# Kernel tuning notes

Measured on AMD Instinct MI355X. Metric: run time of the kernel, lower is better.

## Reference

```python
import jax, jax.numpy as jnp
import numpy as np

H = 128        # num_hidden
NIN = 384      # num_in
FF = 4 * H
SCALE = 30.0
EPS = 1e-5


def _gelu(x):
    return jax.nn.gelu(x, approximate=False)


def _layernorm(x, g, b):
    mu = jnp.mean(x, axis=-1, keepdims=True)
    var = jnp.var(x, axis=-1, keepdims=True)
    return (x - mu) * jax.lax.rsqrt(var + EPS) * g + b


def setup_inputs() -> dict:
    key = jax.random.key(0)
    ks = jax.random.split(key, 12)
    B, N, K = 4, 2048, 48
    s = lambda fan_in: 1.0 / np.sqrt(fan_in)
    inp = {
        "h_V": jax.random.normal(ks[0], (B, N, H), jnp.float32),
        "h_E": jax.random.normal(ks[1], (B, N, K, NIN), jnp.float32),
        "mask_V": jnp.ones((B, N), jnp.float32),
        "mask_attend": jnp.ones((B, N, K), jnp.float32),
        "W1_w": jax.random.uniform(ks[2], (H + NIN, H), jnp.float32, -s(H + NIN), s(H + NIN)),
        "W1_b": jnp.zeros((H,), jnp.float32),
        "W2_w": jax.random.uniform(ks[3], (H, H), jnp.float32, -s(H), s(H)),
        "W2_b": jnp.zeros((H,), jnp.float32),
        "W3_w": jax.random.uniform(ks[4], (H, H), jnp.float32, -s(H), s(H)),
        "W3_b": jnp.zeros((H,), jnp.float32),
        "Win_w": jax.random.uniform(ks[5], (H, FF), jnp.float32, -s(H), s(H)),
        "Win_b": jnp.zeros((FF,), jnp.float32),
        "Wout_w": jax.random.uniform(ks[6], (FF, H), jnp.float32, -s(FF), s(FF)),
        "Wout_b": jnp.zeros((H,), jnp.float32),
        "ln1_g": jnp.ones((H,), jnp.float32),
        "ln1_b": jnp.zeros((H,), jnp.float32),
        "ln2_g": jnp.ones((H,), jnp.float32),
        "ln2_b": jnp.zeros((H,), jnp.float32),
    }
    return inp


def reference(h_V, h_E, mask_V, mask_attend,
              W1_w, W1_b, W2_w, W2_b, W3_w, W3_b,
              Win_w, Win_b, Wout_w, Wout_b,
              ln1_g, ln1_b, ln2_g, ln2_b):
    B, N, K, _ = h_E.shape
    # expand node feats over K neighbors and concat with edge feats -> [B,N,K,H+NIN]
    h_V_expand = jnp.broadcast_to(h_V[:, :, None, :], (B, N, K, h_V.shape[-1]))
    h_EV = jnp.concatenate([h_V_expand, h_E], axis=-1)
    # edge MLP: 3 linears, 2 GELUs
    h_message = _gelu(h_EV @ W1_w + W1_b)
    h_message = _gelu(h_message @ W2_w + W2_b)
    h_message = h_message @ W3_w + W3_b
    h_message = mask_attend[..., None] * h_message
    dh = jnp.sum(h_message, axis=-2) / SCALE  # [B,N,H]
    h = _layernorm(h_V + dh, ln1_g, ln1_b)
    # position-wise FFN
    dh = _gelu(h @ Win_w + Win_b) @ Wout_w + Wout_b
    h = _layernorm(h + dh, ln2_g, ln2_b)
    h = mask_V[..., None] * h
    return h
```

## Files before the change

kernel.cpp:

```cpp
#include <hip/hip_runtime.h>
#include <hip/hip_bf16.h>

#define Hh    128
#define NINc  384
#define KN    48
#define FFd   512
#define NNODE 8192

typedef __attribute__((ext_vector_type(8))) short short8v;
typedef __attribute__((ext_vector_type(4))) float f32x4;

__device__ __forceinline__ short f2bf1(float f){
  union { __hip_bfloat16 h; short s; } c; c.h = __float2bfloat16(f);
  return c.s;
}
__device__ __forceinline__ unsigned pk_bf16(float lo, float hi){
  union { __hip_bfloat162 h; unsigned u; } c;
  c.h = __float22bfloat162_rn(make_float2(lo, hi));
  return c.u;
}

__device__ __forceinline__ float gelu_f(float x){
  float t = 0.7978845608028654f * x * (1.0f + 0.044715f * x * x);
  float e = __expf(2.0f * t);
  return x * (1.0f - 1.0f / (e + 1.0f));
}

__device__ __forceinline__ void bar_lds(){
  asm volatile("s_waitcnt lgkmcnt(0)\n\ts_barrier" ::: "memory");
}

__global__ void prep_weights(const float* __restrict__ W1, const float* __restrict__ W2,
                             const float* __restrict__ W3, const float* __restrict__ Win,
                             const float* __restrict__ Wout,
                             short* __restrict__ w1vT, short* __restrict__ w1p,
                             short* __restrict__ w2p,  short* __restrict__ w3T,
                             short* __restrict__ winT, short* __restrict__ woutT)
{
  int i = blockIdx.x * 256 + threadIdx.x;
  if (i < 16384){ int n = i / 128, k = i % 128; w1vT[i] = f2bf1(W1[k*128 + n]); return; }
  i -= 16384;
  if (i < 49152){
    int n = i / 6144, r = i % 6144;
    int ks = r / 512, r2 = r % 512;
    int lane = r2 / 8, j = r2 % 8;
    int qq = lane >> 4, arow = lane & 15;
    w1p[i] = f2bf1(W1[(128 + ks*32 + qq*8 + j)*128 + n*16 + arow]); return;
  }
  i -= 49152;
  if (i < 16384){
    int n = i / 2048, r = i % 2048;
    int ks = r / 512, r2 = r % 512;
    int lane = r2 / 8, j = r2 % 8;
    int qq = lane >> 4, arow = lane & 15;
    w2p[i] = f2bf1(W2[(ks*32 + qq*8 + j)*128 + n*16 + arow]); return;
  }
  i -= 16384;
  if (i < 16384){ int n = i / 128, k = i % 128; w3T[i] = f2bf1(W3[k*128 + n]); return; }
  i -= 16384;
  if (i < 65536){ int n = i / 128, k = i % 128; winT[i] = f2bf1(Win[k*512 + n]); return; }
  i -= 65536;
  if (i < 65536){ int n = i / 512, k = i % 512; woutT[i] = f2bf1(Wout[k*128 + n]); return; }
}

__global__ __launch_bounds__(256,4) void np_kernel(
    const float* __restrict__ hV, const short* __restrict__ w1vT,
    const float* __restrict__ b1, float* __restrict__ npart)
{
  const int row0 = blockIdx.x * 32;
  const int tid = threadIdx.x, lane = tid & 63, wv = tid >> 6;
  __shared__ __attribute__((aligned(16))) short Xs[32][Hh + 8];

  const float4* src = (const float4*)(hV + (size_t)row0 * Hh);
  #pragma unroll
  for (int j = 0; j < 4; ++j){
    int idx = tid + 256*j;
    int r = idx >> 5, c4 = idx & 31;
    float4 v = src[idx];
    *(uint2*)&Xs[r][c4*4] = make_uint2(pk_bf16(v.x,v.y), pk_bf16(v.z,v.w));
  }
  __syncthreads();

  const int arow = lane & 15, kgrp = (lane >> 4) * 8;
  const int col0 = wv * 32, ccol = lane & 15, crow0 = (lane >> 4) * 4;

  f32x4 acc[2][2];
  #pragma unroll
  for (int m = 0; m < 2; ++m) for (int n = 0; n < 2; ++n) acc[m][n] = (f32x4){0.f,0.f,0.f,0.f};

  const short8v* Bw = (const short8v*)w1vT;
  #pragma unroll
  for (int ks = 0; ks < 4; ++ks){
    int kb = ks*32 + kgrp;
    short8v b0 = Bw[(col0 + arow)*16      + (kb >> 3)];
    short8v b1f = Bw[(col0 + 16 + arow)*16 + (kb >> 3)];
    #pragma unroll
    for (int m = 0; m < 2; ++m){
      short8v a = *(const short8v*)&Xs[m*16 + arow][kb];
      acc[m][0] = __builtin_amdgcn_mfma_f32_16x16x32_bf16(a, b0,  acc[m][0], 0,0,0);
      acc[m][1] = __builtin_amdgcn_mfma_f32_16x16x32_bf16(a, b1f, acc[m][1], 0,0,0);
    }
  }
  #pragma unroll
  for (int m = 0; m < 2; ++m) for (int n = 0; n < 2; ++n){
    int colg = col0 + n*16 + ccol;
    float bb = b1[colg];
    #pragma unroll
    for (int r = 0; r < 4; ++r)
      npart[(size_t)(row0 + m*16 + crow0 + r)*Hh + colg] = acc[m][n][r] + bb;
  }
}

__global__ __launch_bounds__(256,4) void edge_kernel(
    const float* __restrict__ hE,
    const float* __restrict__ maskA, const float* __restrict__ npart,
    const short* __restrict__ w1p, const short* __restrict__ w2p,
    const float* __restrict__ b2,
    float* __restrict__ sbuf, float* __restrict__ smaskbuf)
{
  const int node = blockIdx.x;
  const int tid = threadIdx.x, lane = tid & 63, wv = tid >> 6;
  const int e = lane & 15, q = lane >> 4;
  const int n0 = wv * 32;

  __shared__ __attribute__((aligned(16))) short Et[KN][NINc + 8];
  short (*M1)[136] = (short (*)[136])&Et[0][0];

  const float4* src = (const float4*)(hE + (size_t)node * (KN*NINc));
  float4 pf[6];

  auto LOADC = [&](int c){
    #pragma unroll
    for (int j = 0; j < 6; ++j){
      int idx = tid + 256*j;
      int r = idx >> 5, c4 = idx & 31;
      pf[j] = src[r*96 + c*32 + c4];
    }
  };
  auto STOREC = [&](int c){
    #pragma unroll
    for (int j = 0; j < 6; ++j){
      int idx = tid + 256*j;
      int r = idx >> 5, c4 = idx & 31;
      *(uint2*)&Et[r][c*128 + c4*4] =
        make_uint2(pk_bf16(pf[j].x, pf[j].y), pk_bf16(pf[j].z, pf[j].w));
    }
  };

  const float4 npv0 = *(const float4*)(npart + (size_t)node*Hh + n0 + 4*q);
  const float4 npv1 = *(const float4*)(npart + (size_t)node*Hh + n0 + 16 + 4*q);
  const float4 b2v0 = *(const float4*)(b2 + n0 + 4*q);
  const float4 b2v1 = *(const float4*)(b2 + n0 + 16 + 4*q);
  const float mk0 = maskA[node*KN + e];
  const float mk1 = maskA[node*KN + 16 + e];
  const float mk2 = maskA[node*KN + 32 + e];

  const f32x4 Z = (f32x4){0.f,0.f,0.f,0.f};
  f32x4 a00=Z, a10=Z, a20=Z, a01=Z, a11=Z, a21=Z;
  const short8v* B1 = (const short8v*)w1p;

  auto G1C = [&](int c){
    #pragma unroll
    for (int kk = 0; kk < 4; ++kk){
      int ks = c*4 + kk;
      short8v f0 = B1[((2*wv  )*12 + ks)*64 + lane];
      short8v f1 = B1[((2*wv+1)*12 + ks)*64 + lane];
      int kb = ks*32 + q*8;
      short8v t0 = *(const short8v*)&Et[e][kb];
      short8v t1 = *(const short8v*)&Et[16 + e][kb];
      short8v t2 = *(const short8v*)&Et[32 + e][kb];
      a00 = __builtin_amdgcn_mfma_f32_16x16x32_bf16(f0, t0, a00, 0,0,0);
      a10 = __builtin_amdgcn_mfma_f32_16x16x32_bf16(f0, t1, a10, 0,0,0);
      a20 = __builtin_amdgcn_mfma_f32_16x16x32_bf16(f0, t2, a20, 0,0,0);
      a01 = __builtin_amdgcn_mfma_f32_16x16x32_bf16(f1, t0, a01, 0,0,0);
      a11 = __builtin_amdgcn_mfma_f32_16x16x32_bf16(f1, t1, a11, 0,0,0);
      a21 = __builtin_amdgcn_mfma_f32_16x16x32_bf16(f1, t2, a21, 0,0,0);
    }
  };

  LOADC(0);
  STOREC(0);
  LOADC(1);
  bar_lds();
  G1C(0);
  STOREC(1);
  LOADC(2);
  bar_lds();
  G1C(1);
  STOREC(2);
  bar_lds();
  G1C(2);
  bar_lds();

  #define WR_M(ACC, ET, COLB, BV)  { short4 s;                      \
    s.x = f2bf1(gelu_f(ACC[0] + BV.x));                             \
    s.y = f2bf1(gelu_f(ACC[1] + BV.y));                             \
    s.z = f2bf1(gelu_f(ACC[2] + BV.z));                             \
    s.w = f2bf1(gelu_f(ACC[3] + BV.w));                             \
    *(short4*)&M1[16*ET + e][COLB + 4*q] = s; }

  WR_M(a00, 0, n0,      npv0)  WR_M(a10, 1, n0,      npv0)
  WR_M(a20, 2, n0,      npv0)  WR_M(a01, 0, n0 + 16, npv1)
  WR_M(a11, 1, n0 + 16, npv1)  WR_M(a21, 2, n0 + 16, npv1)
  #undef WR_M
  bar_lds();

  {
    f32x4 c00=Z, c10=Z, c20=Z, c01=Z, c11=Z, c21=Z;
    const short8v* B2f = (const short8v*)w2p;
    #pragma unroll
    for (int ks = 0; ks < 4; ++ks){
      short8v f0 = B2f[((2*wv  )*4 + ks)*64 + lane];
      short8v f1 = B2f[((2*wv+1)*4 + ks)*64 + lane];
      int kb = ks*32 + q*8;
      short8v t0 = *(const short8v*)&M1[e][kb];
      short8v t1 = *(const short8v*)&M1[16 + e][kb];
      short8v t2 = *(const short8v*)&M1[32 + e][kb];
      c00 = __builtin_amdgcn_mfma_f32_16x16x32_bf16(f0, t0, c00, 0,0,0);
      c10 = __builtin_amdgcn_mfma_f32_16x16x32_bf16(f0, t1, c10, 0,0,0);
      c20 = __builtin_amdgcn_mfma_f32_16x16x32_bf16(f0, t2, c20, 0,0,0);
      c01 = __builtin_amdgcn_mfma_f32_16x16x32_bf16(f1, t0, c01, 0,0,0);
      c11 = __builtin_amdgcn_mfma_f32_16x16x32_bf16(f1, t1, c11, 0,0,0);
      c21 = __builtin_amdgcn_mfma_f32_16x16x32_bf16(f1, t2, c21, 0,0,0);
    }
    float sv0[4], sv1[4];
    #pragma unroll
    for (int r = 0; r < 4; ++r){
      sv0[r] = gelu_f(c00[r] + b2v0[r])*mk0 + gelu_f(c10[r] + b2v0[r])*mk1
             + gelu_f(c20[r] + b2v0[r])*mk2;
      sv1[r] = gelu_f(c01[r] + b2v1[r])*mk0 + gelu_f(c11[r] + b2v1[r])*mk1
             + gelu_f(c21[r] + b2v1[r])*mk2;
    }
    float m3 = mk0 + mk1 + mk2;
    #pragma unroll
    for (int s = 1; s <= 8; s <<= 1){
      #pragma unroll
      for (int r = 0; r < 4; ++r){
        sv0[r] += __shfl_xor(sv0[r], s);
        sv1[r] += __shfl_xor(sv1[r], s);
      }
      m3 += __shfl_xor(m3, s);
    }
    if (e == 0){
      *(float4*)(sbuf + (size_t)node*Hh + n0 + 4*q) =
          make_float4(sv0[0], sv0[1], sv0[2], sv0[3]);
      *(float4*)(sbuf + (size_t)node*Hh + n0 + 16 + 4*q) =
          make_float4(sv1[0], sv1[1], sv1[2], sv1[3]);
    }
    if (tid == 0) smaskbuf[node] = m3;
  }
}

__global__ __launch_bounds__(256,2) void ffn2_kernel(
    const float* __restrict__ hV, const float* __restrict__ sbuf,
    const float* __restrict__ smaskbuf, const short* __restrict__ w3T,
    const float* __restrict__ b3,
    const float* __restrict__ ln1g, const float* __restrict__ ln1b,
    const short* __restrict__ winT, const float* __restrict__ bin,
    const short* __restrict__ woutT, const float* __restrict__ bout,
    const float* __restrict__ ln2g, const float* __restrict__ ln2b,
    const float* __restrict__ maskV, float* __restrict__ out)
{
  const int row0 = blockIdx.x * 32;
  const int tid = threadIdx.x, lane = tid & 63, wv = tid >> 6;
  __shared__ __attribute__((aligned(16))) short Xs[32][Hh + 8];
  __shared__ __attribute__((aligned(16))) float Rs[32][Hh + 4];
  __shared__ __attribute__((aligned(16))) short Hs[32][FFd + 8];
  __shared__ float smS[32];

  const int arow = lane & 15, kgrp = (lane >> 4) * 8;
  const int ccol = lane & 15, crow0 = (lane >> 4) * 4;

  {
    const float4* src = (const float4*)(sbuf + (size_t)row0 * Hh);
    #pragma unroll
    for (int j = 0; j < 4; ++j){
      int idx = tid + 256*j;
      int r = idx >> 5, c4 = idx & 31;
      float4 v = src[idx];
      *(uint2*)&Xs[r][c4*4] = make_uint2(pk_bf16(v.x,v.y), pk_bf16(v.z,v.w));
    }
    if (tid < 32) smS[tid] = smaskbuf[row0 + tid];
  }
  __syncthreads();

  {
    f32x4 acc[2][2];
    #pragma unroll
    for (int m = 0; m < 2; ++m) for (int n = 0; n < 2; ++n) acc[m][n] = (f32x4){0.f,0.f,0.f,0.f};
    const short8v* Bw = (const short8v*)w3T;
    const int col0 = wv * 32;
    #pragma unroll
    for (int ks = 0; ks < 4; ++ks){
      int kb = ks*32 + kgrp;
      short8v b0 = Bw[(col0 + arow)*16      + (kb >> 3)];
      short8v b1f = Bw[(col0 + 16 + arow)*16 + (kb >> 3)];
      #pragma unroll
      for (int m = 0; m < 2; ++m){
        short8v a = *(const short8v*)&Xs[m*16 + arow][kb];
        acc[m][0] = __builtin_amdgcn_mfma_f32_16x16x32_bf16(a, b0,  acc[m][0], 0,0,0);
        acc[m][1] = __builtin_amdgcn_mfma_f32_16x16x32_bf16(a, b1f, acc[m][1], 0,0,0);
      }
    }
    #pragma unroll
    for (int m = 0; m < 2; ++m) for (int n = 0; n < 2; ++n){
      int colg = col0 + n*16 + ccol;
      float bb = b3[colg];
      #pragma unroll
      for (int r = 0; r < 4; ++r){
        int rl = m*16 + crow0 + r;
        Rs[rl][colg] = hV[(size_t)(row0 + rl)*Hh + colg]
                     + (acc[m][n][r] + bb*smS[rl]) * (1.0f/30.0f);
      }
    }
  }
  __syncthreads();

  {
    int r = tid >> 3, cb = (tid & 7) * 16;
    float xv[16];
    #pragma unroll
    for (int j = 0; j < 16; ++j) xv[j] = Rs[r][cb + j];
    float sum = 0.f, sq = 0.f;
    #pragma unroll
    for (int j = 0; j < 16; ++j){ sum += xv[j]; sq += xv[j]*xv[j]; }
    #pragma unroll
    for (int d = 1; d < 8; d <<= 1){ sum += __shfl_xor(sum, d); sq += __shfl_xor(sq, d); }
    float mu = sum * (1.0f/128.0f);
    float var = sq * (1.0f/128.0f) - mu*mu;
    float rstd = rsqrtf(var + 1e-5f);
    #pragma unroll
    for (int j = 0; j < 16; ++j){
      int c = cb + j;
      float xn = (xv[j] - mu) * rstd * ln1g[c] + ln1b[c];
      Xs[r][c] = f2bf1(xn);
      Rs[r][c] = xn;
    }
  }
  __syncthreads();

  {
    f32x4 acc[2][8];
    #pragma unroll
    for (int m = 0; m < 2; ++m) for (int n = 0; n < 8; ++n) acc[m][n] = (f32x4){0.f,0.f,0.f,0.f};
    const short8v* Bw = (const short8v*)winT;
    #pragma unroll
    for (int ks = 0; ks < 4; ++ks){
      int kb = ks*32 + kgrp;
      short8v a0 = *(const short8v*)&Xs[arow][kb];
      short8v a1 = *(const short8v*)&Xs[16 + arow][kb];
      #pragma unroll
      for (int n = 0; n < 8; ++n){
        short8v b = Bw[(wv*128 + n*16 + arow)*16 + (kb >> 3)];
        acc[0][n] = __builtin_amdgcn_mfma_f32_16x16x32_bf16(a0,b,acc[0][n],0,0,0);
        acc[1][n] = __builtin_amdgcn_mfma_f32_16x16x32_bf16(a1,b,acc[1][n],0,0,0);
      }
    }
    #pragma unroll
    for (int m = 0; m < 2; ++m) for (int n = 0; n < 8; ++n){
      int colg = wv*128 + n*16 + ccol;
      float bb = bin[colg];
      #pragma unroll
      for (int r = 0; r < 4; ++r)
        Hs[m*16 + crow0 + r][colg] = f2bf1(gelu_f(acc[m][n][r] + bb));
    }
  }
  __syncthreads();

  {
    f32x4 acc[2][2];
    #pragma unroll
    for (int m = 0; m < 2; ++m) for (int n = 0; n < 2; ++n) acc[m][n] = (f32x4){0.f,0.f,0.f,0.f};
    const short8v* Bw = (const short8v*)woutT;
    #pragma unroll
    for (int ks = 0; ks < 16; ++ks){
      int kb = ks*32 + kgrp;
      short8v a0 = *(const short8v*)&Hs[arow][kb];
      short8v a1 = *(const short8v*)&Hs[16 + arow][kb];
      short8v b0 = Bw[(wv*32 + arow)*64      + (kb >> 3)];
      short8v b1f = Bw[(wv*32 + 16 + arow)*64 + (kb >> 3)];
      acc[0][0] = __builtin_amdgcn_mfma_f32_16x16x32_bf16(a0,b0, acc[0][0],0,0,0);
      acc[1][0] = __builtin_amdgcn_mfma_f32_16x16x32_bf16(a1,b0, acc[1][0],0,0,0);
      acc[0][1] = __builtin_amdgcn_mfma_f32_16x16x32_bf16(a0,b1f,acc[0][1],0,0,0);
      acc[1][1] = __builtin_amdgcn_mfma_f32_16x16x32_bf16(a1,b1f,acc[1][1],0,0,0);
    }
    #pragma unroll
    for (int m = 0; m < 2; ++m) for (int n = 0; n < 2; ++n){
      int colg = wv*32 + n*16 + ccol;
      float bb = bout[colg];
      #pragma unroll
      for (int r = 0; r < 4; ++r){
        int rr = m*16 + crow0 + r;
        Rs[rr][colg] = Rs[rr][colg] + acc[m][n][r] + bb;
      }
    }
  }
  __syncthreads();

  {
    int r = tid >> 3, cb = (tid & 7) * 16;
    float xv[16];
    #pragma unroll
    for (int j = 0; j < 16; ++j) xv[j] = Rs[r][cb + j];
    float sum = 0.f, sq = 0.f;
    #pragma unroll
    for (int j = 0; j < 16; ++j){ sum += xv[j]; sq += xv[j]*xv[j]; }
    #pragma unroll
    for (int d = 1; d < 8; d <<= 1){ sum += __shfl_xor(sum, d); sq += __shfl_xor(sq, d); }
    float mu = sum * (1.0f/128.0f);
    float var = sq * (1.0f/128.0f) - mu*mu;
    float rstd = rsqrtf(var + 1e-5f);
    float mv = maskV[row0 + r];
    float* op = out + (size_t)(row0 + r)*Hh + cb;
    #pragma unroll
    for (int j = 0; j < 4; ++j){
      float4 o;
      o.x = ((xv[j*4+0] - mu)*rstd*ln2g[cb+j*4+0] + ln2b[cb+j*4+0]) * mv;
      o.y = ((xv[j*4+1] - mu)*rstd*ln2g[cb+j*4+1] + ln2b[cb+j*4+1]) * mv;
      o.z = ((xv[j*4+2] - mu)*rstd*ln2g[cb+j*4+2] + ln2b[cb+j*4+2]) * mv;
      o.w = ((xv[j*4+3] - mu)*rstd*ln2g[cb+j*4+3] + ln2b[cb+j*4+3]) * mv;
      ((float4*)op)[j] = o;
    }
  }
}

extern "C" void kernel_launch(void* const* d_in, const int* in_sizes, int n_in,
                              void* d_out, int out_size, void* d_ws, size_t ws_size,
                              hipStream_t stream)
{
  const float* hV    = (const float*)d_in[0];
  const float* hE    = (const float*)d_in[1];
  const float* maskV = (const float*)d_in[2];
  const float* maskA = (const float*)d_in[3];
  const float* W1w   = (const float*)d_in[4];
  const float* W1b   = (const float*)d_in[5];
  const float* W2w   = (const float*)d_in[6];
  const float* W2b   = (const float*)d_in[7];
  const float* W3w   = (const float*)d_in[8];
  const float* W3b   = (const float*)d_in[9];
  const float* Winw  = (const float*)d_in[10];
  const float* Winb  = (const float*)d_in[11];
  const float* Woutw = (const float*)d_in[12];
  const float* Woutb = (const float*)d_in[13];
  const float* l1g   = (const float*)d_in[14];
  const float* l1b   = (const float*)d_in[15];
  const float* l2g   = (const float*)d_in[16];
  const float* l2b   = (const float*)d_in[17];

  char* ws = (char*)d_ws;
  size_t off = 0;
  float* npart = (float*)(ws + off); off += (size_t)NNODE * Hh * 4;
  float* sbuf  = (float*)(ws + off); off += (size_t)NNODE * Hh * 4;
  float* smbuf = (float*)(ws + off); off += (size_t)NNODE * 4;
  short* w1vT  = (short*)(ws + off); off += 16384*2;
  short* w1p   = (short*)(ws + off); off += 49152*2;
  short* w2p   = (short*)(ws + off); off += 16384*2;
  short* w3T   = (short*)(ws + off); off += 16384*2;
  short* winT  = (short*)(ws + off); off += 65536*2;
  short* woutT = (short*)(ws + off); off += 65536*2;
  if (ws_size < off) return;

  prep_weights<<<896, 256, 0, stream>>>(W1w, W2w, W3w, Winw, Woutw,
                                        w1vT, w1p, w2p, w3T, winT, woutT);
  np_kernel<<<NNODE/32, 256, 0, stream>>>(hV, w1vT, W1b, npart);
  edge_kernel<<<NNODE, 256, 0, stream>>>(hE, maskA, npart,
                                         w1p, w2p, W2b, sbuf, smbuf);
  ffn2_kernel<<<NNODE/32, 256, 0, stream>>>(hV, sbuf, smbuf, w3T, W3b,
                                            l1g, l1b, winT, Winb, woutT, Woutb,
                                            l2g, l2b, maskV, (float*)d_out);
}
```

Before: 189.2 us.

## Stage edge features in two larger chunks and store neighbor sums as bf16

The edge kernel now loads h_E in two 192-column chunks of 9 float4 per thread instead of three 128-column chunks of 6. This removes one barrier stage and one load/compute handoff, at the cost of more prefetch registers and a shallower overlap pipeline. The per-node aggregated message buffer is also written as bf16 instead of fp32. That halves its write and read traffic, and ffn2 copies it straight into shared memory without converting.

```diff
diff --git a/kernel.cpp b/kernel.cpp
--- a/kernel.cpp
+++ b/kernel.cpp
@@ -116,7 +116,7 @@
     const float* __restrict__ maskA, const float* __restrict__ npart,
     const short* __restrict__ w1p, const short* __restrict__ w2p,
     const float* __restrict__ b2,
-    float* __restrict__ sbuf, float* __restrict__ smaskbuf)
+    short* __restrict__ sbuf, float* __restrict__ smaskbuf)
 {
   const int node = blockIdx.x;
   const int tid = threadIdx.x, lane = tid & 63, wv = tid >> 6;
@@ -127,22 +127,22 @@
   short (*M1)[136] = (short (*)[136])&Et[0][0];
 
   const float4* src = (const float4*)(hE + (size_t)node * (KN*NINc));
-  float4 pf[6];
+  float4 pf[9];
 
   auto LOADC = [&](int c){
     #pragma unroll
-    for (int j = 0; j < 6; ++j){
+    for (int j = 0; j < 9; ++j){
       int idx = tid + 256*j;
-      int r = idx >> 5, c4 = idx & 31;
-      pf[j] = src[r*96 + c*32 + c4];
+      int r = idx / 48, m4 = idx - r*48;
+      pf[j] = src[r*96 + c*48 + m4];
     }
   };
   auto STOREC = [&](int c){
     #pragma unroll
-    for (int j = 0; j < 6; ++j){
+    for (int j = 0; j < 9; ++j){
       int idx = tid + 256*j;
-      int r = idx >> 5, c4 = idx & 31;
-      *(uint2*)&Et[r][c*128 + c4*4] =
+      int r = idx / 48, m4 = idx - r*48;
+      *(uint2*)&Et[r][c*192 + m4*4] =
         make_uint2(pk_bf16(pf[j].x, pf[j].y), pk_bf16(pf[j].z, pf[j].w));
     }
   };
@@ -161,8 +161,8 @@
 
   auto G1C = [&](int c){
     #pragma unroll
-    for (int kk = 0; kk < 4; ++kk){
-      int ks = c*4 + kk;
+    for (int kk = 0; kk < 6; ++kk){
+      int ks = c*6 + kk;
       short8v f0 = B1[((2*wv  )*12 + ks)*64 + lane];
       short8v f1 = B1[((2*wv+1)*12 + ks)*64 + lane];
       int kb = ks*32 + q*8;
@@ -184,12 +184,8 @@
   bar_lds();
   G1C(0);
   STOREC(1);
-  LOADC(2);
   bar_lds();
   G1C(1);
-  STOREC(2);
-  bar_lds();
-  G1C(2);
   bar_lds();
 
   #define WR_M(ACC, ET, COLB, BV)  { short4 s;                      \
@@ -242,17 +238,17 @@
       m3 += __shfl_xor(m3, s);
     }
     if (e == 0){
-      *(float4*)(sbuf + (size_t)node*Hh + n0 + 4*q) =
-          make_float4(sv0[0], sv0[1], sv0[2], sv0[3]);
-      *(float4*)(sbuf + (size_t)node*Hh + n0 + 16 + 4*q) =
-          make_float4(sv1[0], sv1[1], sv1[2], sv1[3]);
+      *(uint2*)(sbuf + (size_t)node*Hh + n0 + 4*q) =
+          make_uint2(pk_bf16(sv0[0], sv0[1]), pk_bf16(sv0[2], sv0[3]));
+      *(uint2*)(sbuf + (size_t)node*Hh + n0 + 16 + 4*q) =
+          make_uint2(pk_bf16(sv1[0], sv1[1]), pk_bf16(sv1[2], sv1[3]));
     }
     if (tid == 0) smaskbuf[node] = m3;
   }
 }
 
 __global__ __launch_bounds__(256,2) void ffn2_kernel(
-    const float* __restrict__ hV, const float* __restrict__ sbuf,
+    const float* __restrict__ hV, const short* __restrict__ sbuf,
     const float* __restrict__ smaskbuf, const short* __restrict__ w3T,
     const float* __restrict__ b3,
     const float* __restrict__ ln1g, const float* __restrict__ ln1b,
@@ -272,13 +268,12 @@
   const int ccol = lane & 15, crow0 = (lane >> 4) * 4;
 
   {
-    const float4* src = (const float4*)(sbuf + (size_t)row0 * Hh);
-    #pragma unroll
-    for (int j = 0; j < 4; ++j){
+    const uint4* src = (const uint4*)(sbuf + (size_t)row0 * Hh);
+    #pragma unroll
+    for (int j = 0; j < 2; ++j){
       int idx = tid + 256*j;
-      int r = idx >> 5, c4 = idx & 31;
-      float4 v = src[idx];
-      *(uint2*)&Xs[r][c4*4] = make_uint2(pk_bf16(v.x,v.y), pk_bf16(v.z,v.w));
+      int r = idx >> 4, c8 = idx & 15;
+      *(uint4*)&Xs[r][c8*8] = src[idx];
     }
     if (tid < 32) smS[tid] = smaskbuf[row0 + tid];
   }
@@ -450,7 +445,7 @@
   char* ws = (char*)d_ws;
   size_t off = 0;
   float* npart = (float*)(ws + off); off += (size_t)NNODE * Hh * 4;
-  float* sbuf  = (float*)(ws + off); off += (size_t)NNODE * Hh * 4;
+  short* sbuf  = (short*)(ws + off); off += (size_t)NNODE * Hh * 2;
   float* smbuf = (float*)(ws + off); off += (size_t)NNODE * 4;
   short* w1vT  = (short*)(ws + off); off += 16384*2;
   short* w1p   = (short*)(ws + off); off += 49152*2;
```

After: 229.8 us. 1.21x slower.
